# Kernel optimization log

Hardware: AMD Instinct MI355X
Metric: run time of the kernel (lower is better)

Reference implementation:

```python
import jax, jax.numpy as jnp
import numpy as np

N, E, IN_DIM, HID, HEADS = 50000, 800000, 128, 16, 8
EPS_BN = 1e-5


def _gat_conv(x, edge_index, W, att_src, att_dst, bias, heads, out_ch, concat):
    # x: [N, F_in]; W: [heads*out_ch, F_in]; att_*: [heads, out_ch]
    n = x.shape[0]
    h = (x @ W.T).reshape(n, heads, out_ch)            # [N, H, C]
    a_src = (h * att_src[None]).sum(-1)                # [N, H]
    a_dst = (h * att_dst[None]).sum(-1)                # [N, H]
    src, dst = edge_index[0], edge_index[1]
    alpha = jax.nn.leaky_relu(a_src[src] + a_dst[dst], negative_slope=0.2)  # [E, H]
    # segment softmax over destination node (per head)
    amax = jax.ops.segment_max(alpha, dst, num_segments=n)
    amax = jnp.where(jnp.isfinite(amax), amax, 0.0)
    ex = jnp.exp(alpha - amax[dst])
    denom = jax.ops.segment_sum(ex, dst, num_segments=n)
    attn = ex / (denom[dst] + 1e-16)                   # [E, H]
    msg = h[src] * attn[:, :, None]                    # [E, H, C]
    out = jax.ops.segment_sum(msg, dst, num_segments=n)  # [N, H, C]
    out = out.reshape(n, heads * out_ch) if concat else out.mean(axis=1)
    return out + bias


def _bn_eval(h, mean, var, gamma, beta):
    return (h - mean) * jax.lax.rsqrt(var + EPS_BN) * gamma + beta


def setup_inputs() -> dict:
    key = jax.random.key(0)
    ks = jax.random.split(key, 16)
    s = 0.1
    inp = {
        "x": jax.random.normal(ks[0], (N, IN_DIM), jnp.float32),
        "edge_index": jax.random.randint(ks[1], (2, E), 0, N, jnp.int32),
        # layer 0: GATConv(128 -> 16, heads=8, concat)
        "w0": jax.random.normal(ks[2], (HEADS * HID, IN_DIM), jnp.float32) * s,
        "asrc0": jax.random.normal(ks[3], (HEADS, HID), jnp.float32) * s,
        "adst0": jax.random.normal(ks[4], (HEADS, HID), jnp.float32) * s,
        "b0": jnp.zeros((HEADS * HID,), jnp.float32),
        "skip0": jax.random.normal(ks[5], (HEADS * HID, IN_DIM), jnp.float32) * s,
        "bn0_g": jnp.ones((HEADS * HID,), jnp.float32),
        "bn0_b": jnp.zeros((HEADS * HID,), jnp.float32),
        "bn0_m": jax.random.normal(ks[6], (HEADS * HID,), jnp.float32) * s,
        "bn0_v": jax.random.uniform(ks[7], (HEADS * HID,), jnp.float32, 0.5, 1.5),
        # layer 1: GATConv(128 -> 16, heads=1, concat=False)
        "w1": jax.random.normal(ks[8], (HID, HEADS * HID), jnp.float32) * s,
        "asrc1": jax.random.normal(ks[9], (1, HID), jnp.float32) * s,
        "adst1": jax.random.normal(ks[10], (1, HID), jnp.float32) * s,
        "b1": jnp.zeros((HID,), jnp.float32),
        "skip1": jax.random.normal(ks[11], (HID, HEADS * HID), jnp.float32) * s,
        "bn1_g": jnp.ones((HID,), jnp.float32),
        "bn1_b": jnp.zeros((HID,), jnp.float32),
        "bn1_m": jax.random.normal(ks[12], (HID,), jnp.float32) * s,
        "bn1_v": jax.random.uniform(ks[13], (HID,), jnp.float32, 0.5, 1.5),
    }
    return inp


def reference(x, edge_index, w0, asrc0, adst0, b0, skip0, bn0_g, bn0_b, bn0_m, bn0_v,
              w1, asrc1, adst1, b1, skip1, bn1_g, bn1_b, bn1_m, bn1_v):
    # eval mode: dropout = identity, BN uses running stats
    h_in = x
    h = _gat_conv(h_in, edge_index, w0, asrc0, adst0, b0, HEADS, HID, True)   # [N, 128]
    h = _bn_eval(h, bn0_m, bn0_v, bn0_g, bn0_b)
    h = h + h_in @ skip0.T
    h = jax.nn.elu(h)
    h_in = h
    h = _gat_conv(h_in, edge_index, w1, asrc1, adst1, b1, 1, HID, False)      # [N, 16]
    h = _bn_eval(h, bn1_m, bn1_v, bn1_g, bn1_b)
    h = h + h_in @ skip1.T
    h = jax.nn.elu(h)
    return h
```

## Files before the change

### kernel.cpp

```cpp
#include <hip/hip_runtime.h>
#include <hip/hip_bf16.h>

#define NN 50000
#define EE 800000
#define INDIM 128
#define HIDC 16
#define NHEAD 8
#define COARSE 196
#define EPB 2048
#define CAPR 6144
#define CAPB 8192
#define CVT_BLKS 37
#define AGG0_BLKS 2048

typedef __attribute__((ext_vector_type(8))) short bf16x8;
typedef __attribute__((ext_vector_type(4))) float f32x4;
typedef __attribute__((ext_vector_type(2))) float f32x2;

#if defined(__has_builtin)
#if __has_builtin(__builtin_amdgcn_cvt_pk_f32_fp8)
#define HAVE_PK_F32_FP8 1
#endif
#endif

__device__ __forceinline__ float bf2f(unsigned short u) {
    union { float f; unsigned int i; } v; v.i = ((unsigned int)u) << 16; return v.f;
}
__device__ __forceinline__ unsigned short f2bf(float f) {
    union { float f; unsigned int i; } v; v.f = f;
    unsigned int r = v.i + 0x7FFFu + ((v.i >> 16) & 1u);
    return (unsigned short)(r >> 16);
}

__global__ __launch_bounds__(256) void k_prep(
    const float* __restrict__ w0, const float* __restrict__ skip0,
    const float* __restrict__ w1, const float* __restrict__ skip1,
    const float* __restrict__ b0, const float* __restrict__ g0,
    const float* __restrict__ bb0, const float* __restrict__ m0,
    const float* __restrict__ v0,
    const float* __restrict__ b1, const float* __restrict__ g1,
    const float* __restrict__ bb1, const float* __restrict__ m1,
    const float* __restrict__ v1,
    unsigned int* __restrict__ wb2, unsigned int* __restrict__ wb1_2,
    float2* __restrict__ acb0, float2* __restrict__ acb1,
    const int* __restrict__ ei, int* __restrict__ ccur0,
    unsigned int* __restrict__ pairs)
{
    if (blockIdx.x < CVT_BLKS) {
        const long NW = 256 * 128 / 4;
        const long NW1 = 32 * 128 / 4;
        long i = (long)blockIdx.x * 256 + threadIdx.x;
        if (i < NW) {
            const float4* src = (i < 128 * 128 / 4) ? ((const float4*)w0 + i)
                                                    : ((const float4*)skip0 + (i - 128 * 128 / 4));
            float4 v = *src;
            wb2[i * 2]     = (unsigned int)f2bf(v.x) | ((unsigned int)f2bf(v.y) << 16);
            wb2[i * 2 + 1] = (unsigned int)f2bf(v.z) | ((unsigned int)f2bf(v.w) << 16);
        } else if (i < NW + NW1) {
            long j = i - NW;
            const float4* src = (j < 16 * 128 / 4) ? ((const float4*)w1 + j)
                                                   : ((const float4*)skip1 + (j - 16 * 128 / 4));
            float4 v = *src;
            wb1_2[j * 2]     = (unsigned int)f2bf(v.x) | ((unsigned int)f2bf(v.y) << 16);
            wb1_2[j * 2 + 1] = (unsigned int)f2bf(v.z) | ((unsigned int)f2bf(v.w) << 16);
        } else if (i < NW + NW1 + 128) {
            int c = (int)(i - NW - NW1);
            float A = g0[c] * rsqrtf(v0[c] + 1e-5f);
            acb0[c] = make_float2(A, (b0[c] - m0[c]) * A + bb0[c]);
        } else if (i < NW + NW1 + 128 + 16) {
            int c = (int)(i - NW - NW1 - 128);
            float A = g1[c] * rsqrtf(v1[c] + 1e-5f);
            acb1[c] = make_float2(A, (b1[c] - m1[c]) * A + bb1[c]);
        }
        return;
    }

    __shared__ int bcnt[256];
    __shared__ int lofs[256];
    __shared__ int gofs[256];
    __shared__ unsigned int stage[EPB];
    __shared__ int gpos[EPB];
    const int t = threadIdx.x;
    const int e0 = (blockIdx.x - CVT_BLKS) * EPB;

    bcnt[t] = 0;
    __syncthreads();

    int mybin[8], myrank[8];
    unsigned int mypair[8];
    #pragma unroll
    for (int k = 0; k < 8; k++) {
        int e = e0 + k * 256 + t;
        mybin[k] = -1;
        if (e < EE) {
            int s = ei[e], d = ei[EE + e];
            int b = d >> 8;
            myrank[k] = atomicAdd(&bcnt[b], 1);
            mybin[k] = b;
            mypair[k] = ((unsigned)d << 16) | (unsigned)s;
        }
    }
    __syncthreads();

    int v = bcnt[t];
    lofs[t] = v;
    __syncthreads();
    for (int off = 1; off < 256; off <<= 1) {
        int u = (t >= off) ? lofs[t - off] : 0;
        __syncthreads();
        lofs[t] += u;
        __syncthreads();
    }
    if (t < COARSE && v > 0)
        gofs[t] = t * CAPR + atomicAdd(&ccur0[t], v);
    __syncthreads();

    #pragma unroll
    for (int k = 0; k < 8; k++) {
        int b = mybin[k];
        if (b >= 0) {
            int slot = (lofs[b] - bcnt[b]) + myrank[k];
            stage[slot] = mypair[k];
            gpos[slot]  = gofs[b] + myrank[k];
        }
    }
    __syncthreads();

    const int total = lofs[255];
    for (int i = t; i < total; i += 256)
        pairs[gpos[i]] = stage[i];
}

__global__ __launch_bounds__(256) void k_mid(
    const unsigned int* __restrict__ pairs, const int* __restrict__ ccur0,
    unsigned short* __restrict__ srcidx, int* __restrict__ rowbeg,
    int* __restrict__ deg,
    const float* __restrict__ x, const unsigned short* __restrict__ wb,
    const float* __restrict__ asrc0, const float* __restrict__ adst0,
    unsigned char* __restrict__ h0f, unsigned short* __restrict__ s0b,
    float* __restrict__ a_src0, float* __restrict__ a_dst0)
{
    __shared__ int fcnt[256], fofs[256], fcur[256];
    __shared__ unsigned short stage[CAPB];

    if (blockIdx.x < COARSE) {
        const int b = blockIdx.x, t = threadIdx.x;
        const int beg = b * CAPR;
        int cnt = ccur0[b];
        if (cnt > CAPR) cnt = CAPR;

        fcnt[t] = 0;
        __syncthreads();
        for (int i = t; i < cnt; i += 256) {
            unsigned int d = pairs[beg + i] >> 16;
            atomicAdd(&fcnt[d & 255], 1);
        }
        __syncthreads();

        int v = fcnt[t];
        fofs[t] = v;
        __syncthreads();
        for (int off = 1; off < 256; off <<= 1) {
            int u = (t >= off) ? fofs[t - off] : 0;
            __syncthreads();
            fofs[t] += u;
            __syncthreads();
        }
        int ex = fofs[t] - v;
        int node = b * 256 + t;
        if (node < NN) { rowbeg[node] = beg + ex; deg[node] = v; }
        fcur[t] = ex;
        __syncthreads();

        for (int i = t; i < cnt; i += 256) {
            unsigned int p = pairs[beg + i];
            unsigned int d = p >> 16;
            int slot = atomicAdd(&fcur[d & 255], 1);
            stage[slot] = (unsigned short)(p & 0xFFFFu);
        }
        __syncthreads();
        for (int i = t; i < cnt; i += 256)
            srcidx[beg + i] = stage[i];
        return;
    }

    const int bid = blockIdx.x - COARSE;
    const int wave = threadIdx.x >> 6;
    const int lane = threadIdx.x & 63;
    const int lrow = lane & 15;
    const int quad = lane >> 4;
    const int rowbase = bid * 32;

    bf16x8 afrag[2][4];
    #pragma unroll
    for (int sub = 0; sub < 2; sub++) {
        const int row = min(rowbase + sub * 16 + lrow, NN - 1);
        const float* xr = x + (long)row * 128;
        #pragma unroll
        for (int ki = 0; ki < 4; ki++) {
            float4 a = *(const float4*)(xr + ki * 32 + quad * 8);
            float4 b = *(const float4*)(xr + ki * 32 + quad * 8 + 4);
            bf16x8 f;
            f[0] = (short)f2bf(a.x); f[1] = (short)f2bf(a.y);
            f[2] = (short)f2bf(a.z); f[3] = (short)f2bf(a.w);
            f[4] = (short)f2bf(b.x); f[5] = (short)f2bf(b.y);
            f[6] = (short)f2bf(b.z); f[7] = (short)f2bf(b.w);
            afrag[sub][ki] = f;
        }
    }

    #pragma unroll
    for (int t = 0; t < 4; t++) {
        const int jg = wave * 64 + t * 16 + lrow;
        bf16x8 bfrag[4];
        #pragma unroll
        for (int ki = 0; ki < 4; ki++)
            bfrag[ki] = *(const bf16x8*)(wb + (long)jg * 128 + ki * 32 + quad * 8);
        float4 asv = {0.f, 0.f, 0.f, 0.f}, adv = {0.f, 0.f, 0.f, 0.f};
        if (wave < 2) {
            const int cb = wave * 64 + t * 16 + quad * 4;
            asv = *(const float4*)(asrc0 + cb);
            adv = *(const float4*)(adst0 + cb);
        }
        #pragma unroll
        for (int sub = 0; sub < 2; sub++) {
            f32x4 acc = (f32x4){0.f, 0.f, 0.f, 0.f};
            #pragma unroll
            for (int ki = 0; ki < 4; ki++)
                acc = __builtin_amdgcn_mfma_f32_16x16x32_bf16(bfrag[ki], afrag[sub][ki], acc, 0, 0, 0);

            const int node = rowbase + sub * 16 + lrow;
            if (node < NN) {
                if (wave < 2) {
                    const int cb = wave * 64 + t * 16 + quad * 4;
                    unsigned int u = __builtin_amdgcn_cvt_pk_fp8_f32(acc[0], acc[1], 0u, 0);
                    u = __builtin_amdgcn_cvt_pk_fp8_f32(acc[2], acc[3], u, 1);
                    *(unsigned int*)(h0f + (long)node * 128 + cb) = u;
                    float ps = acc[0] * asv.x + acc[1] * asv.y + acc[2] * asv.z + acc[3] * asv.w;
                    float pd = acc[0] * adv.x + acc[1] * adv.y + acc[2] * adv.z + acc[3] * adv.w;
                    ps += __shfl_xor(ps, 16); ps += __shfl_xor(ps, 32);
                    pd += __shfl_xor(pd, 16); pd += __shfl_xor(pd, 32);
                    if (quad == 0) {
                        const int h = wave * 4 + t;
                        a_src0[(long)node * 8 + h] = ps;
                        a_dst0[(long)node * 8 + h] = pd;
                    }
                } else {
                    const int cb = (wave - 2) * 64 + t * 16 + quad * 4;
                    uint2 u;
                    u.x = (unsigned int)f2bf(acc[0]) | ((unsigned int)f2bf(acc[1]) << 16);
                    u.y = (unsigned int)f2bf(acc[2]) | ((unsigned int)f2bf(acc[3]) << 16);
                    *(uint2*)(s0b + (long)node * 128 + cb) = u;
                }
            }
        }
    }
}

__global__ __launch_bounds__(256) void k_agg0(
    const int* __restrict__ rowbeg, const int* __restrict__ deg,
    const unsigned short* __restrict__ srcidx,
    const unsigned char* __restrict__ h0f, const float* __restrict__ a_src0,
    const float* __restrict__ a_dst0, const unsigned short* __restrict__ s0b,
    const float2* __restrict__ acb0, unsigned short* __restrict__ hab)
{
    const int wid = (blockIdx.x * 256 + threadIdx.x) >> 6;
    const int nwaves = AGG0_BLKS * 4;
    const int lane = threadIdx.x & 63;
    const int l16 = lane & 15;
    const int c0 = l16 * 8;
    const int hsel = l16 >> 1;
    const int q = lane >> 4;

    for (int d = wid; d < NN; d += nwaves) {
        const int beg = rowbeg[d], end = beg + deg[d];
        const float adst = a_dst0[d * 8 + hsel];

        float den = 0.f;
        f32x2 acc2[4] = {(f32x2){0.f, 0.f}, (f32x2){0.f, 0.f},
                         (f32x2){0.f, 0.f}, (f32x2){0.f, 0.f}};
        for (int i = beg; i < end; i += 16) {
            int ss[4];
            float ww[4];
            #pragma unroll
            for (int k = 0; k < 4; k++) {
                const int e = i + k * 4 + q;
                const bool v = e < end;
                const int s = v ? (int)srcidx[e] : 0;
                float a = a_src0[s * 8 + hsel] + adst;
                a = a > 0.f ? a : 0.2f * a;
                ww[k] = v ? __expf(a) : 0.f;
                ss[k] = s;
                den += ww[k];
            }
            #pragma unroll
            for (int k = 0; k < 4; k++) {
                const uint2 u = *(const uint2*)(h0f + ((unsigned)ss[k] << 7) + c0);
                const float w = ww[k];
#ifdef HAVE_PK_F32_FP8
                acc2[0] += w * __builtin_amdgcn_cvt_pk_f32_fp8((int)u.x, false);
                acc2[1] += w * __builtin_amdgcn_cvt_pk_f32_fp8((int)u.x, true);
                acc2[2] += w * __builtin_amdgcn_cvt_pk_f32_fp8((int)u.y, false);
                acc2[3] += w * __builtin_amdgcn_cvt_pk_f32_fp8((int)u.y, true);
#else
                acc2[0][0] += w * __builtin_amdgcn_cvt_f32_fp8(u.x, 0);
                acc2[0][1] += w * __builtin_amdgcn_cvt_f32_fp8(u.x, 1);
                acc2[1][0] += w * __builtin_amdgcn_cvt_f32_fp8(u.x, 2);
                acc2[1][1] += w * __builtin_amdgcn_cvt_f32_fp8(u.x, 3);
                acc2[2][0] += w * __builtin_amdgcn_cvt_f32_fp8(u.y, 0);
                acc2[2][1] += w * __builtin_amdgcn_cvt_f32_fp8(u.y, 1);
                acc2[3][0] += w * __builtin_amdgcn_cvt_f32_fp8(u.y, 2);
                acc2[3][1] += w * __builtin_amdgcn_cvt_f32_fp8(u.y, 3);
#endif
            }
        }
        den += __shfl_xor(den, 1);
        den += __shfl_xor(den, 16);
        den += __shfl_xor(den, 32);
        den *= 0.5f;
        #pragma unroll
        for (int p = 0; p < 4; p++) {
            acc2[p][0] += __shfl_xor(acc2[p][0], 16);
            acc2[p][0] += __shfl_xor(acc2[p][0], 32);
            acc2[p][1] += __shfl_xor(acc2[p][1], 16);
            acc2[p][1] += __shfl_xor(acc2[p][1], 32);
        }

        if (q == 0) {
            const float inv = 1.f / (den + 1e-16f);
            const float4* abf = (const float4*)((const float*)acb0 + 2 * c0);
            const uint4 su = *(const uint4*)(s0b + (long)d * 128 + c0);
            const unsigned int sw[4] = {su.x, su.y, su.z, su.w};
            unsigned int res[4];
            #pragma unroll
            for (int p = 0; p < 4; p++) {
                const float4 ab = abf[p];
                float x0 = acc2[p][0] * inv * ab.x + ab.y + bf2f((unsigned short)sw[p]);
                float x1 = acc2[p][1] * inv * ab.z + ab.w + bf2f((unsigned short)(sw[p] >> 16));
                x0 = x0 > 0.f ? x0 : __expf(x0) - 1.f;
                x1 = x1 > 0.f ? x1 : __expf(x1) - 1.f;
                res[p] = (unsigned int)f2bf(x0) | ((unsigned int)f2bf(x1) << 16);
            }
            *(uint4*)(hab + (long)d * 128 + c0) = make_uint4(res[0], res[1], res[2], res[3]);
        }
    }
}

__global__ __launch_bounds__(256) void k_post0(
    const unsigned short* __restrict__ hab,
    const unsigned short* __restrict__ wb1,
    const float* __restrict__ asrc1, const float* __restrict__ adst1,
    unsigned short* __restrict__ h1b, float* __restrict__ s1,
    float* __restrict__ a_src1, float* __restrict__ a_dst1)
{
    const int tid = threadIdx.x;
    const int lane = tid & 63, wave = tid >> 6;
    const int lrow = lane & 15, quad = lane >> 4;

    bf16x8 bfrag[2][4];
    #pragma unroll
    for (int t = 0; t < 2; t++)
        #pragma unroll
        for (int ki = 0; ki < 4; ki++)
            bfrag[t][ki] = *(const bf16x8*)(wb1 + (long)(t * 16 + lrow) * 128 + ki * 32 + quad * 8);
    const float avec = asrc1[lrow];
    const float dvec = adst1[lrow];

    const int tile = blockIdx.x * 4 + wave;
    if (tile * 16 >= NN) return;
    const int n0 = tile * 16;
    const long arow = (long)(n0 + lrow) * 128;

    bf16x8 afrag[4];
    #pragma unroll
    for (int ki = 0; ki < 4; ki++)
        afrag[ki] = *(const bf16x8*)(hab + arow + ki * 32 + quad * 8);

    f32x4 acc0 = (f32x4){0.f, 0.f, 0.f, 0.f};
    f32x4 acc1 = (f32x4){0.f, 0.f, 0.f, 0.f};
    #pragma unroll
    for (int ki = 0; ki < 4; ki++) {
        acc0 = __builtin_amdgcn_mfma_f32_16x16x32_bf16(afrag[ki], bfrag[0][ki], acc0, 0, 0, 0);
        acc1 = __builtin_amdgcn_mfma_f32_16x16x32_bf16(afrag[ki], bfrag[1][ki], acc1, 0, 0, 0);
    }

    #pragma unroll
    for (int r = 0; r < 4; r++) {
        const int node = n0 + quad * 4 + r;
        h1b[(long)node * 16 + lrow] = f2bf(acc0[r]);
        s1[(long)node * 16 + lrow] = acc1[r];
        float ps = acc0[r] * avec;
        float pd = acc0[r] * dvec;
        ps += __shfl_xor(ps, 1); ps += __shfl_xor(ps, 2);
        ps += __shfl_xor(ps, 4); ps += __shfl_xor(ps, 8);
        pd += __shfl_xor(pd, 1); pd += __shfl_xor(pd, 2);
        pd += __shfl_xor(pd, 4); pd += __shfl_xor(pd, 8);
        if (lrow == 0) { a_src1[node] = ps; a_dst1[node] = pd; }
    }
}

__global__ __launch_bounds__(256) void k_agg1_final(
    const int* __restrict__ rowbeg, const int* __restrict__ deg,
    const unsigned short* __restrict__ srcidx,
    const unsigned short* __restrict__ h1b, const float* __restrict__ a_src1,
    const float* __restrict__ a_dst1, const float* __restrict__ s1,
    const float2* __restrict__ acb1, float* __restrict__ out)
{
    const int gid = blockIdx.x * 256 + threadIdx.x;
    const int d = gid >> 3;
    if (d >= NN) return;
    const int lane = threadIdx.x & 63;
    const int gl = lane & 7;
    const int c0 = (gl & 1) * 8;
    const int q = gl >> 1;
    const int beg = rowbeg[d], end = beg + deg[d];
    const float adst = a_dst1[d];

    float den = 0.f;
    float acc[8] = {0.f, 0.f, 0.f, 0.f, 0.f, 0.f, 0.f, 0.f};
    for (int i = beg; i < end; i += 16) {
        int ss[4];
        float ww[4];
        #pragma unroll
        for (int k = 0; k < 4; k++) {
            const int e = i + k * 4 + q;
            const bool v = e < end;
            const int s = v ? (int)srcidx[e] : 0;
            float a = a_src1[s] + adst;
            a = a > 0.f ? a : 0.2f * a;
            ww[k] = v ? __expf(a) : 0.f;
            ss[k] = s;
            den += ww[k];
        }
        #pragma unroll
        for (int k = 0; k < 4; k++) {
            const uint4 u = *(const uint4*)(h1b + ss[k] * 16 + c0);
            const float w = ww[k];
            acc[0] += w * bf2f((unsigned short)u.x);
            acc[1] += w * bf2f((unsigned short)(u.x >> 16));
            acc[2] += w * bf2f((unsigned short)u.y);
            acc[3] += w * bf2f((unsigned short)(u.y >> 16));
            acc[4] += w * bf2f((unsigned short)u.z);
            acc[5] += w * bf2f((unsigned short)(u.z >> 16));
            acc[6] += w * bf2f((unsigned short)u.w);
            acc[7] += w * bf2f((unsigned short)(u.w >> 16));
        }
    }
    den += __shfl_xor(den, 1);
    den += __shfl_xor(den, 2);
    den += __shfl_xor(den, 4);
    den *= 0.5f;
    #pragma unroll
    for (int p = 0; p < 8; p++) {
        acc[p] += __shfl_xor(acc[p], 2);
        acc[p] += __shfl_xor(acc[p], 4);
    }

    if (q == 0) {
        const float inv = 1.f / (den + 1e-16f);
        const float4* abf = (const float4*)((const float*)acb1 + 2 * c0);
        const float4 sv0 = *(const float4*)(s1 + (long)d * 16 + c0);
        const float4 sv1 = *(const float4*)(s1 + (long)d * 16 + c0 + 4);
        const float svf[8] = {sv0.x, sv0.y, sv0.z, sv0.w, sv1.x, sv1.y, sv1.z, sv1.w};
        float o[8];
        #pragma unroll
        for (int p = 0; p < 4; p++) {
            const float4 ab = abf[p];
            float v0o = acc[2 * p]     * inv * ab.x + ab.y + svf[2 * p];
            float v1o = acc[2 * p + 1] * inv * ab.z + ab.w + svf[2 * p + 1];
            o[2 * p]     = v0o > 0.f ? v0o : __expf(v0o) - 1.f;
            o[2 * p + 1] = v1o > 0.f ? v1o : __expf(v1o) - 1.f;
        }
        *(float4*)(out + (long)d * 16 + c0)     = make_float4(o[0], o[1], o[2], o[3]);
        *(float4*)(out + (long)d * 16 + c0 + 4) = make_float4(o[4], o[5], o[6], o[7]);
    }
}

extern "C" void kernel_launch(void* const* d_in, const int* in_sizes, int n_in,
                              void* d_out, int out_size, void* d_ws, size_t ws_size,
                              hipStream_t stream)
{
    (void)in_sizes; (void)n_in; (void)out_size; (void)ws_size;
    const float* x     = (const float*)d_in[0];
    const int*   ei    = (const int*)d_in[1];
    const float* w0    = (const float*)d_in[2];
    const float* asrc0 = (const float*)d_in[3];
    const float* adst0 = (const float*)d_in[4];
    const float* b0    = (const float*)d_in[5];
    const float* skip0 = (const float*)d_in[6];
    const float* bn0g  = (const float*)d_in[7];
    const float* bn0b  = (const float*)d_in[8];
    const float* bn0m  = (const float*)d_in[9];
    const float* bn0v  = (const float*)d_in[10];
    const float* w1    = (const float*)d_in[11];
    const float* asrc1 = (const float*)d_in[12];
    const float* adst1 = (const float*)d_in[13];
    const float* b1    = (const float*)d_in[14];
    const float* skip1 = (const float*)d_in[15];
    const float* bn1g  = (const float*)d_in[16];
    const float* bn1b  = (const float*)d_in[17];
    const float* bn1m  = (const float*)d_in[18];
    const float* bn1v  = (const float*)d_in[19];

    const long NPAIR = (long)COARSE * CAPR;
    unsigned int* pairs = (unsigned int*)d_ws;
    unsigned short* wb    = (unsigned short*)(pairs + NPAIR);
    unsigned short* wb1   = wb + 256 * 128;
    unsigned short* s0b   = wb1 + 32 * 128;
    unsigned short* hab   = s0b + (long)NN * 128;
    unsigned short* h1b   = hab + (long)NN * 128;
    unsigned short* srcidx= h1b + (long)NN * 16;
    unsigned char*  h0f   = (unsigned char*)(srcidx + NPAIR);
    float* a_src0 = (float*)(h0f + (long)NN * 128);
    float* a_dst0 = a_src0 + (long)NN * 8;
    float* s1     = a_dst0 + (long)NN * 8;
    float* a_src1 = s1 + (long)NN * 16;
    float* a_dst1 = a_src1 + NN;
    float2* acb0  = (float2*)(a_dst1 + NN);
    float2* acb1  = acb0 + 128;
    int* ccur0  = (int*)(acb1 + 16);
    int* rowbeg = ccur0 + COARSE;
    int* deg    = rowbeg + NN;

    hipMemsetAsync(ccur0, 0, (size_t)COARSE * 4, stream);

    const int PREP_BLKS = CVT_BLKS + (EE + EPB - 1) / EPB;
    k_prep<<<PREP_BLKS, 256, 0, stream>>>(
        w0, skip0, w1, skip1,
        b0, bn0g, bn0b, bn0m, bn0v, b1, bn1g, bn1b, bn1m, bn1v,
        (unsigned int*)wb, (unsigned int*)wb1, acb0, acb1,
        ei, ccur0, pairs);

    const int MID_BLKS = COARSE + (NN + 31) / 32;
    k_mid<<<MID_BLKS, 256, 0, stream>>>(
        pairs, ccur0, srcidx, rowbeg, deg,
        x, wb, asrc0, adst0, h0f, s0b, a_src0, a_dst0);

    k_agg0<<<AGG0_BLKS, 256, 0, stream>>>(rowbeg, deg, srcidx, h0f,
                                          a_src0, a_dst0, s0b, acb0,
                                          hab);
    k_post0<<<(NN / 16 + 3) / 4, 256, 0, stream>>>(hab, wb1, asrc1, adst1,
                                                   h1b, s1, a_src1, a_dst1);
    k_agg1_final<<<(NN * 8 + 255) / 256, 256, 0, stream>>>(rowbeg, deg, srcidx, h1b,
                                                           a_src1, a_dst1, s1,
                                                           acb1, (float*)d_out);
}
```

Measured before the change: 219.4 us.

## Process two destination nodes per wave and dedupe edge-weight math via shuffles

Both aggregation kernels now handle two destination nodes per wave (or per 8-lane group) and walk their edge lists together up to the longer degree. In layer 0, each lane computes attention weights for one (edge, head) pair and broadcasts them with shuffles, so exp/leaky-relu is no longer computed redundantly across lanes. This gives more gathers in flight per wave and removes duplicated exponentials. The cost is more registers, extra shuffles, and wasted iterations when the two nodes' degrees differ.

Result: faster. 210.4 us (-4.1%).

```diff
diff --git a/kernel.cpp b/kernel.cpp
--- a/kernel.cpp
+++ b/kernel.cpp
@@ -267,81 +267,162 @@
     const int wid = (blockIdx.x * 256 + threadIdx.x) >> 6;
     const int nwaves = AGG0_BLKS * 4;
     const int lane = threadIdx.x & 63;
+    const int eslot = lane >> 3;
+    const int hph1 = lane & 7;
     const int l16 = lane & 15;
     const int c0 = l16 * 8;
     const int hsel = l16 >> 1;
     const int q = lane >> 4;
 
-    for (int d = wid; d < NN; d += nwaves) {
-        const int beg = rowbeg[d], end = beg + deg[d];
-        const float adst = a_dst0[d * 8 + hsel];
-
-        float den = 0.f;
-        f32x2 acc2[4] = {(f32x2){0.f, 0.f}, (f32x2){0.f, 0.f},
+    for (int dd = wid; dd < NN / 2; dd += nwaves) {
+        const int X = dd * 2, Y = X + 1;
+        const int begX = rowbeg[X], endX = begX + deg[X];
+        const int begY = rowbeg[Y], endY = begY + deg[Y];
+        const float adX = a_dst0[X * 8 + hph1];
+        const float adY = a_dst0[Y * 8 + hph1];
+
+        float denX = 0.f, denY = 0.f;
+        f32x2 accX[4] = {(f32x2){0.f, 0.f}, (f32x2){0.f, 0.f},
                          (f32x2){0.f, 0.f}, (f32x2){0.f, 0.f}};
-        for (int i = beg; i < end; i += 16) {
-            int ss[4];
-            float ww[4];
+        f32x2 accY[4] = {(f32x2){0.f, 0.f}, (f32x2){0.f, 0.f},
+                         (f32x2){0.f, 0.f}, (f32x2){0.f, 0.f}};
+        const int nb = max(endX - begX, endY - begY);
+        for (int off = 0; off < nb; off += 16) {
+            const int xA = begX + off + eslot, xB = xA + 8;
+            const int yA = begY + off + eslot, yB = yA + 8;
+            const bool vXA = xA < endX, vXB = xB < endX;
+            const bool vYA = yA < endY, vYB = yB < endY;
+            const int sXA = vXA ? (int)srcidx[xA] : 0;
+            const int sXB = vXB ? (int)srcidx[xB] : 0;
+            const int sYA = vYA ? (int)srcidx[yA] : 0;
+            const int sYB = vYB ? (int)srcidx[yB] : 0;
+            float aXA = a_src0[sXA * 8 + hph1] + adX;
+            float aXB = a_src0[sXB * 8 + hph1] + adX;
+            float aYA = a_src0[sYA * 8 + hph1] + adY;
+            float aYB = a_src0[sYB * 8 + hph1] + adY;
+            aXA = aXA > 0.f ? aXA : 0.2f * aXA;
+            aXB = aXB > 0.f ? aXB : 0.2f * aXB;
+            aYA = aYA > 0.f ? aYA : 0.2f * aYA;
+            aYB = aYB > 0.f ? aYB : 0.2f * aYB;
+            const float wXA = vXA ? __expf(aXA) : 0.f;
+            const float wXB = vXB ? __expf(aXB) : 0.f;
+            const float wYA = vYA ? __expf(aYA) : 0.f;
+            const float wYB = vYB ? __expf(aYB) : 0.f;
+            denX += wXA + wXB;
+            denY += wYA + wYB;
             #pragma unroll
-            for (int k = 0; k < 4; k++) {
-                const int e = i + k * 4 + q;
-                const bool v = e < end;
-                const int s = v ? (int)srcidx[e] : 0;
-                float a = a_src0[s * 8 + hsel] + adst;
-                a = a > 0.f ? a : 0.2f * a;
-                ww[k] = v ? __expf(a) : 0.f;
-                ss[k] = s;
-                den += ww[k];
-            }
-            #pragma unroll
-            for (int k = 0; k < 4; k++) {
-                const uint2 u = *(const uint2*)(h0f + ((unsigned)ss[k] << 7) + c0);
-                const float w = ww[k];
+            for (int kk = 0; kk < 2; kk++) {
+                const int k8 = (kk * 4 + q) * 8;
+                const float wxa = __shfl(wXA, k8 + hsel);
+                const int   sxa = __shfl(sXA, k8);
+                const float wxb = __shfl(wXB, k8 + hsel);
+                const int   sxb = __shfl(sXB, k8);
+                const float wya = __shfl(wYA, k8 + hsel);
+                const int   sya = __shfl(sYA, k8);
+                const float wyb = __shfl(wYB, k8 + hsel);
+                const int   syb = __shfl(sYB, k8);
+                const uint2 uxa = *(const uint2*)(h0f + ((unsigned)sxa << 7) + c0);
+                const uint2 uxb = *(const uint2*)(h0f + ((unsigned)sxb << 7) + c0);
+                const uint2 uya = *(const uint2*)(h0f + ((unsigned)sya << 7) + c0);
+                const uint2 uyb = *(const uint2*)(h0f + ((unsigned)syb << 7) + c0);
 #ifdef HAVE_PK_F32_FP8
-                acc2[0] += w * __builtin_amdgcn_cvt_pk_f32_fp8((int)u.x, false);
-                acc2[1] += w * __builtin_amdgcn_cvt_pk_f32_fp8((int)u.x, true);
-                acc2[2] += w * __builtin_amdgcn_cvt_pk_f32_fp8((int)u.y, false);
-                acc2[3] += w * __builtin_amdgcn_cvt_pk_f32_fp8((int)u.y, true);
+                accX[0] += wxa * __builtin_amdgcn_cvt_pk_f32_fp8((int)uxa.x, false)
+                         + wxb * __builtin_amdgcn_cvt_pk_f32_fp8((int)uxb.x, false);
+                accX[1] += wxa * __builtin_amdgcn_cvt_pk_f32_fp8((int)uxa.x, true)
+                         + wxb * __builtin_amdgcn_cvt_pk_f32_fp8((int)uxb.x, true);
+                accX[2] += wxa * __builtin_amdgcn_cvt_pk_f32_fp8((int)uxa.y, false)
+                         + wxb * __builtin_amdgcn_cvt_pk_f32_fp8((int)uxb.y, false);
+                accX[3] += wxa * __builtin_amdgcn_cvt_pk_f32_fp8((int)uxa.y, true)
+                         + wxb * __builtin_amdgcn_cvt_pk_f32_fp8((int)uxb.y, true);
+                accY[0] += wya * __builtin_amdgcn_cvt_pk_f32_fp8((int)uya.x, false)
+                         + wyb * __builtin_amdgcn_cvt_pk_f32_fp8((int)uyb.x, false);
+                accY[1] += wya * __builtin_amdgcn_cvt_pk_f32_fp8((int)uya.x, true)
+                         + wyb * __builtin_amdgcn_cvt_pk_f32_fp8((int)uyb.x, true);
+                accY[2] += wya * __builtin_amdgcn_cvt_pk_f32_fp8((int)uya.y, false)
+                         + wyb * __builtin_amdgcn_cvt_pk_f32_fp8((int)uyb.y, false);
+                accY[3] += wya * __builtin_amdgcn_cvt_pk_f32_fp8((int)uya.y, true)
+                         + wyb * __builtin_amdgcn_cvt_pk_f32_fp8((int)uyb.y, true);
 #else
-                acc2[0][0] += w * __builtin_amdgcn_cvt_f32_fp8(u.x, 0);
-                acc2[0][1] += w * __builtin_amdgcn_cvt_f32_fp8(u.x, 1);
-                acc2[1][0] += w * __builtin_amdgcn_cvt_f32_fp8(u.x, 2);
-                acc2[1][1] += w * __builtin_amdgcn_cvt_f32_fp8(u.x, 3);
-                acc2[2][0] += w * __builtin_amdgcn_cvt_f32_fp8(u.y, 0);
-                acc2[2][1] += w * __builtin_amdgcn_cvt_f32_fp8(u.y, 1);
-                acc2[3][0] += w * __builtin_amdgcn_cvt_f32_fp8(u.y, 2);
-                acc2[3][1] += w * __builtin_amdgcn_cvt_f32_fp8(u.y, 3);
+                accX[0][0] += wxa * __builtin_amdgcn_cvt_f32_fp8(uxa.x, 0)
+                            + wxb * __builtin_amdgcn_cvt_f32_fp8(uxb.x, 0);
+                accX[0][1] += wxa * __builtin_amdgcn_cvt_f32_fp8(uxa.x, 1)
+                            + wxb * __builtin_amdgcn_cvt_f32_fp8(uxb.x, 1);
+                accX[1][0] += wxa * __builtin_amdgcn_cvt_f32_fp8(uxa.x, 2)
+                            + wxb * __builtin_amdgcn_cvt_f32_fp8(uxb.x, 2);
+                accX[1][1] += wxa * __builtin_amdgcn_cvt_f32_fp8(uxa.x, 3)
+                            + wxb * __builtin_amdgcn_cvt_f32_fp8(uxb.x, 3);
+                accX[2][0] += wxa * __builtin_amdgcn_cvt_f32_fp8(uxa.y, 0)
+                            + wxb * __builtin_amdgcn_cvt_f32_fp8(uxb.y, 0);
+                accX[2][1] += wxa * __builtin_amdgcn_cvt_f32_fp8(uxa.y, 1)
+                            + wxb * __builtin_amdgcn_cvt_f32_fp8(uxb.y, 1);
+                accX[3][0] += wxa * __builtin_amdgcn_cvt_f32_fp8(uxa.y, 2)
+                            + wxb * __builtin_amdgcn_cvt_f32_fp8(uxb.y, 2);
+                accX[3][1] += wxa * __builtin_amdgcn_cvt_f32_fp8(uxa.y, 3)
+                            + wxb * __builtin_amdgcn_cvt_f32_fp8(uxb.y, 3);
+                accY[0][0] += wya * __builtin_amdgcn_cvt_f32_fp8(uya.x, 0)
+                            + wyb * __builtin_amdgcn_cvt_f32_fp8(uyb.x, 0);
+                accY[0][1] += wya * __builtin_amdgcn_cvt_f32_fp8(uya.x, 1)
+                            + wyb * __builtin_amdgcn_cvt_f32_fp8(uyb.x, 1);
+                accY[1][0] += wya * __builtin_amdgcn_cvt_f32_fp8(uya.x, 2)
+                            + wyb * __builtin_amdgcn_cvt_f32_fp8(uyb.x, 2);
+                accY[1][1] += wya * __builtin_amdgcn_cvt_f32_fp8(uya.x, 3)
+                            + wyb * __builtin_amdgcn_cvt_f32_fp8(uyb.x, 3);
+                accY[2][0] += wya * __builtin_amdgcn_cvt_f32_fp8(uya.y, 0)
+                            + wyb * __builtin_amdgcn_cvt_f32_fp8(uyb.y, 0);
+                accY[2][1] += wya * __builtin_amdgcn_cvt_f32_fp8(uya.y, 1)
+                            + wyb * __builtin_amdgcn_cvt_f32_fp8(uyb.y, 1);
+                accY[3][0] += wya * __builtin_amdgcn_cvt_f32_fp8(uya.y, 2)
+                            + wyb * __builtin_amdgcn_cvt_f32_fp8(uyb.y, 2);
+                accY[3][1] += wya * __builtin_amdgcn_cvt_f32_fp8(uya.y, 3)
+                            + wyb * __builtin_amdgcn_cvt_f32_fp8(uyb.y, 3);
 #endif
             }
         }
-        den += __shfl_xor(den, 1);
-        den += __shfl_xor(den, 16);
-        den += __shfl_xor(den, 32);
-        den *= 0.5f;
+        denX += __shfl_xor(denX, 8);
+        denX += __shfl_xor(denX, 16);
+        denX += __shfl_xor(denX, 32);
+        denY += __shfl_xor(denY, 8);
+        denY += __shfl_xor(denY, 16);
+        denY += __shfl_xor(denY, 32);
+        const float dhX = __shfl(denX, hsel);
+        const float dhY = __shfl(denY, hsel);
         #pragma unroll
         for (int p = 0; p < 4; p++) {
-            acc2[p][0] += __shfl_xor(acc2[p][0], 16);
-            acc2[p][0] += __shfl_xor(acc2[p][0], 32);
-            acc2[p][1] += __shfl_xor(acc2[p][1], 16);
-            acc2[p][1] += __shfl_xor(acc2[p][1], 32);
+            accX[p][0] += __shfl_xor(accX[p][0], 16);
+            accX[p][0] += __shfl_xor(accX[p][0], 32);
+            accX[p][1] += __shfl_xor(accX[p][1], 16);
+            accX[p][1] += __shfl_xor(accX[p][1], 32);
+            accY[p][0] += __shfl_xor(accY[p][0], 16);
+            accY[p][0] += __shfl_xor(accY[p][0], 32);
+            accY[p][1] += __shfl_xor(accY[p][1], 16);
+            accY[p][1] += __shfl_xor(accY[p][1], 32);
         }
 
         if (q == 0) {
-            const float inv = 1.f / (den + 1e-16f);
+            const float invX = 1.f / (dhX + 1e-16f);
+            const float invY = 1.f / (dhY + 1e-16f);
             const float4* abf = (const float4*)((const float*)acb0 + 2 * c0);
-            const uint4 su = *(const uint4*)(s0b + (long)d * 128 + c0);
-            const unsigned int sw[4] = {su.x, su.y, su.z, su.w};
-            unsigned int res[4];
+            const uint4 suX = *(const uint4*)(s0b + (long)X * 128 + c0);
+            const uint4 suY = *(const uint4*)(s0b + (long)Y * 128 + c0);
+            const unsigned int swX[4] = {suX.x, suX.y, suX.z, suX.w};
+            const unsigned int swY[4] = {suY.x, suY.y, suY.z, suY.w};
+            unsigned int resX[4], resY[4];
             #pragma unroll
             for (int p = 0; p < 4; p++) {
                 const float4 ab = abf[p];
-                float x0 = acc2[p][0] * inv * ab.x + ab.y + bf2f((unsigned short)sw[p]);
-                float x1 = acc2[p][1] * inv * ab.z + ab.w + bf2f((unsigned short)(sw[p] >> 16));
+                float x0 = accX[p][0] * invX * ab.x + ab.y + bf2f((unsigned short)swX[p]);
+                float x1 = accX[p][1] * invX * ab.z + ab.w + bf2f((unsigned short)(swX[p] >> 16));
+                float y0 = accY[p][0] * invY * ab.x + ab.y + bf2f((unsigned short)swY[p]);
+                float y1 = accY[p][1] * invY * ab.z + ab.w + bf2f((unsigned short)(swY[p] >> 16));
                 x0 = x0 > 0.f ? x0 : __expf(x0) - 1.f;
                 x1 = x1 > 0.f ? x1 : __expf(x1) - 1.f;
-                res[p] = (unsigned int)f2bf(x0) | ((unsigned int)f2bf(x1) << 16);
+                y0 = y0 > 0.f ? y0 : __expf(y0) - 1.f;
+                y1 = y1 > 0.f ? y1 : __expf(y1) - 1.f;
+                resX[p] = (unsigned int)f2bf(x0) | ((unsigned int)f2bf(x1) << 16);
+                resY[p] = (unsigned int)f2bf(y0) | ((unsigned int)f2bf(y1) << 16);
             }
-            *(uint4*)(hab + (long)d * 128 + c0) = make_uint4(res[0], res[1], res[2], res[3]);
+            *(uint4*)(hab + (long)X * 128 + c0) = make_uint4(resX[0], resX[1], resX[2], resX[3]);
+            *(uint4*)(hab + (long)Y * 128 + c0) = make_uint4(resY[0], resY[1], resY[2], resY[3]);
         }
     }
 }
@@ -406,73 +487,117 @@
     const float* __restrict__ a_dst1, const float* __restrict__ s1,
     const float2* __restrict__ acb1, float* __restrict__ out)
 {
-    const int gid = blockIdx.x * 256 + threadIdx.x;
-    const int d = gid >> 3;
-    if (d >= NN) return;
+    const int g = (blockIdx.x * 256 + threadIdx.x) >> 3;
+    const int X = g * 2, Y = X + 1;
+    if (X >= NN) return;
     const int lane = threadIdx.x & 63;
     const int gl = lane & 7;
+    const int gb = lane & ~7;
     const int c0 = (gl & 1) * 8;
     const int q = gl >> 1;
-    const int beg = rowbeg[d], end = beg + deg[d];
-    const float adst = a_dst1[d];
-
-    float den = 0.f;
-    float acc[8] = {0.f, 0.f, 0.f, 0.f, 0.f, 0.f, 0.f, 0.f};
-    for (int i = beg; i < end; i += 16) {
-        int ss[4];
-        float ww[4];
+    const int begX = rowbeg[X], endX = begX + deg[X];
+    const int begY = rowbeg[Y], endY = begY + deg[Y];
+    const float adX = a_dst1[X];
+    const float adY = a_dst1[Y];
+
+    float denX = 0.f, denY = 0.f;
+    float accX[8] = {0.f, 0.f, 0.f, 0.f, 0.f, 0.f, 0.f, 0.f};
+    float accY[8] = {0.f, 0.f, 0.f, 0.f, 0.f, 0.f, 0.f, 0.f};
+    const int nb = max(endX - begX, endY - begY);
+    for (int off = 0; off < nb; off += 16) {
+        const int xA = begX + off + gl, xB = xA + 8;
+        const int yA = begY + off + gl, yB = yA + 8;
+        const bool vXA = xA < endX, vXB = xB < endX;
+        const bool vYA = yA < endY, vYB = yB < endY;
+        const int sXA = vXA ? (int)srcidx[xA] : 0;
+        const int sXB = vXB ? (int)srcidx[xB] : 0;
+        const int sYA = vYA ? (int)srcidx[yA] : 0;
+        const int sYB = vYB ? (int)srcidx[yB] : 0;
+        float aXA = a_src1[sXA] + adX;
+        float aXB = a_src1[sXB] + adX;
+        float aYA = a_src1[sYA] + adY;
+        float aYB = a_src1[sYB] + adY;
+        aXA = aXA > 0.f ? aXA : 0.2f * aXA;
+        aXB = aXB > 0.f ? aXB : 0.2f * aXB;
+        aYA = aYA > 0.f ? aYA : 0.2f * aYA;
+        aYB = aYB > 0.f ? aYB : 0.2f * aYB;
+        const float wXA = vXA ? __expf(aXA) : 0.f;
+        const float wXB = vXB ? __expf(aXB) : 0.f;
+        const float wYA = vYA ? __expf(aYA) : 0.f;
+        const float wYB = vYB ? __expf(aYB) : 0.f;
+        denX += wXA + wXB;
+        denY += wYA + wYB;
         #pragma unroll
-        for (int k = 0; k < 4; k++) {
-            const int e = i + k * 4 + q;
-            const bool v = e < end;
-            const int s = v ? (int)srcidx[e] : 0;
-            float a = a_src1[s] + adst;
-            a = a > 0.f ? a : 0.2f * a;
-            ww[k] = v ? __expf(a) : 0.f;
-            ss[k] = s;
-            den += ww[k];
-        }
-        #pragma unroll
-        for (int k = 0; k < 4; k++) {
-            const uint4 u = *(const uint4*)(h1b + ss[k] * 16 + c0);
-            const float w = ww[k];
-            acc[0] += w * bf2f((unsigned short)u.x);
-            acc[1] += w * bf2f((unsigned short)(u.x >> 16));
-            acc[2] += w * bf2f((unsigned short)u.y);
-            acc[3] += w * bf2f((unsigned short)(u.y >> 16));
-            acc[4] += w * bf2f((unsigned short)u.z);
-            acc[5] += w * bf2f((unsigned short)(u.z >> 16));
-            acc[6] += w * bf2f((unsigned short)u.w);
-            acc[7] += w * bf2f((unsigned short)(u.w >> 16));
-        }
-    }
-    den += __shfl_xor(den, 1);
-    den += __shfl_xor(den, 2);
-    den += __shfl_xor(den, 4);
-    den *= 0.5f;
+        for (int kk = 0; kk < 2; kk++) {
+            const int k = kk * 4 + q;
+            const float wxa = __shfl(wXA, gb | k);
+            const int   sxa = __shfl(sXA, gb | k);
+            const float wxb = __shfl(wXB, gb | k);
+            const int   sxb = __shfl(sXB, gb | k);
+            const float wya = __shfl(wYA, gb | k);
+            const int   sya = __shfl(sYA, gb | k);
+            const float wyb = __shfl(wYB, gb | k);
+            const int   syb = __shfl(sYB, gb | k);
+            const uint4 uxa = *(const uint4*)(h1b + sxa * 16 + c0);
+            const uint4 uxb = *(const uint4*)(h1b + sxb * 16 + c0);
+            const uint4 uya = *(const uint4*)(h1b + sya * 16 + c0);
+            const uint4 uyb = *(const uint4*)(h1b + syb * 16 + c0);
+            const unsigned int ux[8] = {uxa.x, uxa.y, uxa.z, uxa.w, uxb.x, uxb.y, uxb.z, uxb.w};
+            const unsigned int uy[8] = {uya.x, uya.y, uya.z, uya.w, uyb.x, uyb.y, uyb.z, uyb.w};
+            #pragma unroll
+            for (int p = 0; p < 4; p++) {
+                accX[2 * p]     += wxa * bf2f((unsigned short)ux[p]);
+                accX[2 * p + 1] += wxa * bf2f((unsigned short)(ux[p] >> 16));
+                accX[2 * p]     += wxb * bf2f((unsigned short)ux[p + 4]);
+                accX[2 * p + 1] += wxb * bf2f((unsigned short)(ux[p + 4] >> 16));
+                accY[2 * p]     += wya * bf2f((unsigned short)uy[p]);
+                accY[2 * p + 1] += wya * bf2f((unsigned short)(uy[p] >> 16));
+                accY[2 * p]     += wyb * bf2f((unsigned short)uy[p + 4]);
+                accY[2 * p + 1] += wyb * bf2f((unsigned short)(uy[p + 4] >> 16));
+            }
+        }
+    }
+    denX += __shfl_xor(denX, 1);
+    denX += __shfl_xor(denX, 2);
+    denX += __shfl_xor(denX, 4);
+    denY += __shfl_xor(denY, 1);
+    denY += __shfl_xor(denY, 2);
+    denY += __shfl_xor(denY, 4);
     #pragma unroll
     for (int p = 0; p < 8; p++) {
-        acc[p] += __shfl_xor(acc[p], 2);
-        acc[p] += __shfl_xor(acc[p], 4);
+        accX[p] += __shfl_xor(accX[p], 2);
+        accX[p] += __shfl_xor(accX[p], 4);
+        accY[p] += __shfl_xor(accY[p], 2);
+        accY[p] += __shfl_xor(accY[p], 4);
     }
 
     if (q == 0) {
-        const float inv = 1.f / (den + 1e-16f);
+        const float invX = 1.f / (denX + 1e-16f);
+        const float invY = 1.f / (denY + 1e-16f);
         const float4* abf = (const float4*)((const float*)acb1 + 2 * c0);
-        const float4 sv0 = *(const float4*)(s1 + (long)d * 16 + c0);
-        const float4 sv1 = *(const float4*)(s1 + (long)d * 16 + c0 + 4);
-        const float svf[8] = {sv0.x, sv0.y, sv0.z, sv0.w, sv1.x, sv1.y, sv1.z, sv1.w};
-        float o[8];
+        const float4 svX0 = *(const float4*)(s1 + (long)X * 16 + c0);
+        const float4 svX1 = *(const float4*)(s1 + (long)X * 16 + c0 + 4);
+        const float4 svY0 = *(const float4*)(s1 + (long)Y * 16 + c0);
+        const float4 svY1 = *(const float4*)(s1 + (long)Y * 16 + c0 + 4);
+        const float sfX[8] = {svX0.x, svX0.y, svX0.z, svX0.w, svX1.x, svX1.y, svX1.z, svX1.w};
+        const float sfY[8] = {svY0.x, svY0.y, svY0.z, svY0.w, svY1.x, svY1.y, svY1.z, svY1.w};
+        float oX[8], oY[8];
         #pragma unroll
         for (int p = 0; p < 4; p++) {
             const float4 ab = abf[p];
-            float v0o = acc[2 * p]     * inv * ab.x + ab.y + svf[2 * p];
-            float v1o = acc[2 * p + 1] * inv * ab.z + ab.w + svf[2 * p + 1];
-            o[2 * p]     = v0o > 0.f ? v0o : __expf(v0o) - 1.f;
-            o[2 * p + 1] = v1o > 0.f ? v1o : __expf(v1o) - 1.f;
-        }
-        *(float4*)(out + (long)d * 16 + c0)     = make_float4(o[0], o[1], o[2], o[3]);
-        *(float4*)(out + (long)d * 16 + c0 + 4) = make_float4(o[4], o[5], o[6], o[7]);
+            float x0 = accX[2 * p]     * invX * ab.x + ab.y + sfX[2 * p];
+            float x1 = accX[2 * p + 1] * invX * ab.z + ab.w + sfX[2 * p + 1];
+            float y0 = accY[2 * p]     * invY * ab.x + ab.y + sfY[2 * p];
+            float y1 = accY[2 * p + 1] * invY * ab.z + ab.w + sfY[2 * p + 1];
+            oX[2 * p]     = x0 > 0.f ? x0 : __expf(x0) - 1.f;
+            oX[2 * p + 1] = x1 > 0.f ? x1 : __expf(x1) - 1.f;
+            oY[2 * p]     = y0 > 0.f ? y0 : __expf(y0) - 1.f;
+            oY[2 * p + 1] = y1 > 0.f ? y1 : __expf(y1) - 1.f;
+        }
+        *(float4*)(out + (long)X * 16 + c0)     = make_float4(oX[0], oX[1], oX[2], oX[3]);
+        *(float4*)(out + (long)X * 16 + c0 + 4) = make_float4(oX[4], oX[5], oX[6], oX[7]);
+        *(float4*)(out + (long)Y * 16 + c0)     = make_float4(oY[0], oY[1], oY[2], oY[3]);
+        *(float4*)(out + (long)Y * 16 + c0 + 4) = make_float4(oY[4], oY[5], oY[6], oY[7]);
     }
 }
 
@@ -541,7 +666,7 @@
                                           hab);
     k_post0<<<(NN / 16 + 3) / 4, 256, 0, stream>>>(hab, wb1, asrc1, adst1,
                                                    h1b, s1, a_src1, a_dst1);
-    k_agg1_final<<<(NN * 8 + 255) / 256, 256, 0, stream>>>(rowbeg, deg, srcidx, h1b,
-                                                           a_src1, a_dst1, s1,
-                                                           acb1, (float*)d_out);
-}
+    k_agg1_final<<<(NN / 2 * 8 + 255) / 256, 256, 0, stream>>>(rowbeg, deg, srcidx, h1b,
+                                                               a_src1, a_dst1, s1,
+                                                               acb1, (float*)d_out);
+}
```
